# Kernel optimization log

Measured on AMD Instinct MI355X. Metric: run time of the kernel, lower is better.

Reference implementation:

```python
import jax, jax.numpy as jnp
import numpy as np

EMG_SAMPLE_RATE = 2000
ROLLOUT_FREQ = 50
LEFT_CTX = 32
RIGHT_CTX = 32
NUM_POSITION_STEPS = 2000  # in EMG samples
OUT_CH = 20


def _interp_linear(x, size, align_corners):
    """x: [..., L] -> [..., size]; matches torch F.interpolate(mode='linear')."""
    L = x.shape[-1]
    if align_corners:
        src = jnp.arange(size, dtype=jnp.float32) * ((L - 1) / max(size - 1, 1))
    else:
        src = (jnp.arange(size, dtype=jnp.float32) + 0.5) * (L / size) - 0.5
        src = jnp.clip(src, 0.0, L - 1)
    lo = jnp.floor(src).astype(jnp.int32)
    hi = jnp.minimum(lo + 1, L - 1)
    w = (src - lo.astype(jnp.float32)).astype(x.dtype)
    return x[..., lo] * (1 - w) + x[..., hi] * w


def setup_inputs() -> dict:
    key = jax.random.key(0)
    ks = jax.random.split(key, 8)
    B, C, T = 32, 16, 8000
    F, K, H = 512, 65, 512
    emg = jax.random.normal(ks[0], (B, C, T), jnp.float32)
    joint_angles = jax.random.normal(ks[1], (B, OUT_CH, T), jnp.float32)
    no_ik_failure = jnp.ones((B, T), dtype=bool)
    conv_w = jax.random.normal(ks[2], (F, C, K), jnp.float32) * 0.05
    conv_b = jnp.zeros((F,), jnp.float32)
    w1 = jax.random.normal(ks[3], (F + OUT_CH, H), jnp.float32) * 0.04
    b1 = jnp.zeros((H,), jnp.float32)
    w2 = jax.random.normal(ks[4], (H, 2 * OUT_CH), jnp.float32) * 0.04
    b2 = jnp.zeros((2 * OUT_CH,), jnp.float32)
    return dict(emg=emg, joint_angles=joint_angles, no_ik_failure=no_ik_failure,
                provide_initial_pos=1, conv_w=conv_w, conv_b=conv_b,
                w1=w1, b1=b1, w2=w2, b2=b2)


def reference(emg, joint_angles, no_ik_failure, provide_initial_pos,
              conv_w, conv_b, w1, b1, w2, b2):
    B, _, T = emg.shape
    initial_pos = joint_angles[:, :, LEFT_CTX]
    if not provide_initial_pos:
        initial_pos = jnp.zeros_like(initial_pos)

    # encoder: valid Conv1d -> [B, F, T - K + 1] = [B, F, T - 64]
    feats = jax.lax.conv_general_dilated(
        emg, conv_w, window_strides=(1,), padding='VALID',
        dimension_numbers=('NCH', 'OIH', 'NCH')) + conv_b[None, :, None]

    seconds = (T - LEFT_CTX - RIGHT_CTX) / EMG_SAMPLE_RATE
    n_time = round(seconds * ROLLOUT_FREQ)          # static python int
    feats = _interp_linear(feats, n_time, align_corners=True)  # [B, F, n_time]
    num_pos_steps = round(NUM_POSITION_STEPS * (ROLLOUT_FREQ / EMG_SAMPLE_RATE))

    feats_t = jnp.transpose(feats, (2, 0, 1))  # [n_time, B, F]

    def step(prev, inp):
        x_t, t = inp
        # state_condition=True: concat previous pose prediction
        h = jax.nn.relu(jnp.concatenate([x_t, prev], axis=-1) @ w1 + b1)
        out = h @ w2 + b2                       # [B, 2*OUT_CH]
        pos, vel = out[:, :OUT_CH], out[:, OUT_CH:]
        pred = jnp.where(t < num_pos_steps, pos, prev + vel)
        return pred, pred

    _, preds = jax.lax.scan(step, initial_pos,
                            (feats_t, jnp.arange(n_time)))
    pred = jnp.transpose(preds, (1, 2, 0))  # [B, OUT_CH, n_time]

    ja = joint_angles[:, :, LEFT_CTX:T - RIGHT_CTX]
    mask = no_ik_failure[:, LEFT_CTX:T - RIGHT_CTX]
    nt = ja.shape[-1]
    pred_up = _interp_linear(pred, nt, align_corners=False)
    # nearest resample of mask to its own length is identity
    return pred_up, ja, mask
```

## Files before the change

kernel.cpp:

```cpp
#include <hip/hip_runtime.h>

#define NT   198
#define BB   32
#define CC   16
#define TT   8000
#define FF   512
#define KW   65
#define HD   512
#define OUT  20
#define CJ   (CC*KW)
#define KP   1056
#define MM   (NT*BB)
#define TOUT 7936
#define NPS  50

typedef float f4 __attribute__((ext_vector_type(4)));

#define WS_CW 0
#define WS_BX (WS_CW + KP*HD)
#define WS_X  (WS_BX + HD)
#define WS_PR (WS_X  + MM*HD)
#define WS_ET (WS_PR + MM*OUT)
#define WS_W2T (WS_ET + KP*MM)

#define ESPAN 2688
__global__ __launch_bounds__(256) void k_e2(const float* __restrict__ emg,
                                            float* __restrict__ Et) {
    const int bx = blockIdx.x;
    const int tc = blockIdx.y;
    const int tid = threadIdx.x;
    if (bx >= BB * CC) {
        int idx = (bx - BB * CC) * 3 + tc;
        f4* zp = (f4*)(Et + (size_t)CJ * MM);
        f4 z = {0.f, 0.f, 0.f, 0.f};
        for (int j = tid; j < 2112; j += 256) zp[(size_t)idx * 2112 + j] = z;
        return;
    }
    __shared__ float lds_e[ESPAN];
    const int bq = bx >> 4, c = bx & 15;
    const int t0 = tc * 66;
    const float CSTEP = 7935.0f / 197.0f;
    const int elo0 = (int)floorf((float)t0 * CSTEP);
    const float* erow = emg + (size_t)(bq * CC + c) * TT;
    for (int i = tid; i < ESPAN; i += 256) {
        int g = elo0 + i;
        lds_e[i] = erow[(g < TT) ? g : (TT - 1)];
    }
    __syncthreads();
    for (int o = tid; o < 65 * 66; o += 256) {
        int j = o / 66;
        int tl = o - j * 66;
        int t = t0 + tl;
        float src = (float)t * CSTEP;
        float fl = floorf(src);
        int lo = (int)fl;
        float w = src - fl;
        int dhi = (w > 0.f && lo < TOUT - 1) ? 1 : 0;
        int li = lo - elo0 + j;
        float v = (1.0f - w) * lds_e[li] + w * lds_e[li + dhi];
        Et[(size_t)(c * KW + j) * MM + bq * NT + t] = v;
    }
}

__global__ __launch_bounds__(256) void k_cw2(const float* __restrict__ cwraw,
                                             const float* __restrict__ w1,
                                             float* __restrict__ CW) {
    __shared__ float As[32][68];
    __shared__ float Bs[32][68];
    const int m0 = blockIdx.x * 64;
    const int n0 = blockIdx.y * 64;
    const int tid = threadIdx.x;
    const int tx = tid & 15, ty = tid >> 4;
    const int am = tid & 63;
    const int kb8 = (tid >> 6) * 8;
    const int mrow = m0 + am;
    const int mclamp = mrow < CJ ? mrow : CJ - 1;

    f4 acc[4] = {};
    for (int k0 = 0; k0 < FF; k0 += 32) {
        __syncthreads();
        #pragma unroll
        for (int s = 0; s < 8; ++s)
            As[kb8 + s][am] = cwraw[(size_t)(k0 + kb8 + s) * CJ + mclamp];
        {
            int kb = tid >> 4, c4 = tid & 15;
            *(f4*)&Bs[kb][c4 * 4]      = *(const f4*)(w1 + (size_t)(k0 + kb) * HD + n0 + c4 * 4);
            *(f4*)&Bs[kb + 16][c4 * 4] = *(const f4*)(w1 + (size_t)(k0 + kb + 16) * HD + n0 + c4 * 4);
        }
        __syncthreads();
        #pragma unroll
        for (int kk = 0; kk < 32; ++kk) {
            f4 a = *(f4*)&As[kk][ty * 4];
            f4 bq = *(f4*)&Bs[kk][tx * 4];
            acc[0] += a[0] * bq; acc[1] += a[1] * bq;
            acc[2] += a[2] * bq; acc[3] += a[3] * bq;
        }
    }
    #pragma unroll
    for (int i = 0; i < 4; ++i) {
        int r = m0 + ty * 4 + i;
        if (r < CJ) {
            *(f4*)(CW + (size_t)r * HD + n0 + tx * 4) = acc[i];
        } else if (r < KP) {
            f4 z = {0.f, 0.f, 0.f, 0.f};
            *(f4*)(CW + (size_t)r * HD + n0 + tx * 4) = z;
        }
    }
}

__global__ __launch_bounds__(256) void k_small2(const float* __restrict__ conv_b,
                                                const float* __restrict__ w1,
                                                const float* __restrict__ b1,
                                                const float* __restrict__ w2,
                                                float* __restrict__ bX,
                                                float* __restrict__ w2t) {
    int bid = blockIdx.x, tid = threadIdx.x;
    if (bid < 2) {
        int h = bid * 256 + tid;
        float acc = b1[h];
        for (int f = 0; f < FF; ++f) acc += conv_b[f] * w1[f * HD + h];
        bX[h] = acc;
    } else {
        int q = bid - 2;
        w2t[(size_t)q * HD + tid]       = w2[(size_t)tid * (2 * OUT) + q];
        w2t[(size_t)q * HD + 256 + tid] = w2[(size_t)(256 + tid) * (2 * OUT) + q];
    }
}

__global__ __launch_bounds__(128) void k_x9(const float* __restrict__ Et,
                                            const float* __restrict__ CW,
                                            const float* __restrict__ bX,
                                            float* __restrict__ X0,
                                            float* __restrict__ X1,
                                            float* __restrict__ X2,
                                            float* __restrict__ X3) {
    __shared__ float As[32][68];
    __shared__ float Bs0[32][68];
    __shared__ float Bs1[32][68];
    const int m0 = blockIdx.x * 64;
    const int n0 = blockIdx.y * 128;
    const int kc = blockIdx.z;
    const int kbase = kc * 256;
    const int NK = (kc == 3) ? 9 : 8;
    const int tid = threadIdx.x;
    const int tm = tid >> 4;
    const int tn = tid & 15;
    const int akr = tid >> 4;
    const int ag  = tid & 15;
    const int bkr = tid >> 5;
    const int bg  = tid & 31;

    f4 acc0[8] = {}, acc1[8] = {};

    for (int kt = 0; kt < NK; ++kt) {
        const int k0 = kbase + kt * 32;
        __syncthreads();
        #pragma unroll
        for (int s = 0; s < 4; ++s) {
            f4 v = *(const f4*)(Et + (size_t)(k0 + akr + 8 * s) * MM + m0 + ag * 4);
            *(f4*)&As[akr + 8 * s][ag * 4] = v;
        }
        #pragma unroll
        for (int s = 0; s < 8; ++s) {
            int kr = bkr + 4 * s;
            f4 v = *(const f4*)(CW + (size_t)(k0 + kr) * HD + n0 + bg * 4);
            if (bg < 16) *(f4*)&Bs0[kr][bg * 4] = v;
            else         *(f4*)&Bs1[kr][(bg - 16) * 4] = v;
        }
        __syncthreads();
        #pragma unroll
        for (int kk = 0; kk < 32; ++kk) {
            f4 a0 = *(const f4*)&As[kk][tm * 8];
            f4 a1 = *(const f4*)&As[kk][tm * 8 + 4];
            f4 b0 = *(const f4*)&Bs0[kk][tn * 4];
            f4 b1 = *(const f4*)&Bs1[kk][tn * 4];
            #pragma unroll
            for (int i = 0; i < 4; ++i) {
                acc0[i]     += a0[i] * b0;  acc1[i]     += a0[i] * b1;
                acc0[i + 4] += a1[i] * b0;  acc1[i + 4] += a1[i] * b1;
            }
        }
    }

    float* Xo = (kc == 0) ? X0 : (kc == 1) ? X1 : (kc == 2) ? X2 : X3;
    if (kc == 0) {
        f4 bx0 = *(const f4*)(bX + n0 + tn * 4);
        f4 bx1 = *(const f4*)(bX + n0 + 64 + tn * 4);
        #pragma unroll
        for (int i = 0; i < 8; ++i) {
            size_t off = (size_t)(m0 + 8 * tm + i) * HD + n0;
            *(f4*)(Xo + off + tn * 4)      = acc0[i] + bx0;
            *(f4*)(Xo + off + 64 + tn * 4) = acc1[i] + bx1;
        }
    } else {
        #pragma unroll
        for (int i = 0; i < 8; ++i) {
            size_t off = (size_t)(m0 + 8 * tm + i) * HD + n0;
            *(f4*)(Xo + off + tn * 4)      = acc0[i];
            *(f4*)(Xo + off + 64 + tn * 4) = acc1[i];
        }
    }
}

__global__ __launch_bounds__(256) void k_sum(float* __restrict__ X0,
                                             const float* __restrict__ X1,
                                             const float* __restrict__ X2,
                                             const float* __restrict__ X3) {
    size_t i = (size_t)blockIdx.x * 256 + threadIdx.x;
    f4 a = ((const f4*)X0)[i];
    f4 b = ((const f4*)X1)[i];
    f4 c = ((const f4*)X2)[i];
    f4 d = ((const f4*)X3)[i];
    ((f4*)X0)[i] = (a + b) + (c + d);
}

#define DPPADD(x, ctrl) ((x) + __int_as_float(__builtin_amdgcn_mov_dpp(__float_as_int(x), (ctrl), 0xf, 0xf, true)))

#define SCAN_STEP(T, ISPOS) { \
    if (aown) { \
        int tp = (T) + 2; if (tp > NT - 1) tp = NT - 1; \
        float2 xf = *(const float2*)(Xr + (size_t)tp * HD); \
        f4 pp[5]; \
        _Pragma("unroll") \
        for (int g = 0; g < 5; ++g) pp[g] = *(const f4*)&prev_lds[(T) & 1][g * 4]; \
        float h0 = xc.x, h1 = xc.y; \
        _Pragma("unroll") \
        for (int j = 0; j < OUT; ++j) { \
            float pj = pp[j >> 2][j & 3]; \
            h0 = fmaf(pj, w1p[j].x, h0); h1 = fmaf(pj, w1p[j].y, h1); } \
        h0 = fmaxf(h0, 0.f); h1 = fmaxf(h1, 0.f); \
        float2 hw; hw.x = h0; hw.y = h1; \
        *(float2*)&h_lds[(T) & 1][tid >> 4][(2 * tid) & 31] = hw; \
        xc = xn; xn = xf; \
    } \
    __syncthreads(); \
    f4 a = {0.f, 0.f, 0.f, 0.f}; \
    _Pragma("unroll") \
    for (int s = 0; s < 8; ++s) { \
        f4 hv = *(const f4*)&h_lds[(T) & 1][r][s * 4]; \
        a += hv * ((ISPOS) ? wqp[s] : wqv[s]); } \
    float sum = (a[0] + a[1]) + (a[2] + a[3]); \
    sum = DPPADD(sum, 0xB1);    \
    sum = DPPADD(sum, 0x4E);    \
    sum = DPPADD(sum, 0x141);   \
    sum = DPPADD(sum, 0x140);   \
    float outv = sum + ((ISPOS) ? b2p : b2v); \
    myq = (ISPOS) ? outv : (myq + outv); \
    if (r == 0) { \
        predrow[(size_t)(T) * OUT + q] = myq; \
        prev_lds[((T) + 1) & 1][q] = myq; } \
    __syncthreads(); }

__global__ __launch_bounds__(320, 1) void k_scan(
        const float* __restrict__ X, const float* __restrict__ w1,
        const float* __restrict__ w2t, const float* __restrict__ b2,
        const float* __restrict__ jang, const int* __restrict__ provide,
        float* __restrict__ preds) {
    __shared__ float h_lds[2][16][36];
    __shared__ __align__(16) float prev_lds[2][20];
    const int b = blockIdx.x;
    const int tid = threadIdx.x;
    const int q = tid >> 4;
    const int r = tid & 15;
    const bool aown = tid < 256;

    float2 w1p[OUT];
    if (aown) {
        #pragma unroll
        for (int j = 0; j < OUT; ++j)
            w1p[j] = *(const float2*)(w1 + (size_t)(FF + j) * HD + 2 * tid);
    }
    f4 wqp[8], wqv[8];
    #pragma unroll
    for (int s = 0; s < 8; ++s) {
        wqp[s] = *(const f4*)(w2t + (size_t)q * HD + r * 32 + s * 4);
        wqv[s] = *(const f4*)(w2t + (size_t)(OUT + q) * HD + r * 32 + s * 4);
    }
    float b2p = b2[q], b2v = b2[OUT + q];

    float pvf = provide[0] ? 1.0f : 0.0f;
    float myq = pvf * jang[(size_t)(b * OUT + q) * TT + 32];
    if (r == 0) prev_lds[0][q] = myq;

    const float* Xr = X + (size_t)b * NT * HD + 2 * tid;
    float* predrow = preds + (size_t)b * NT * OUT;
    float2 xc = {0.f, 0.f}, xn = {0.f, 0.f};
    if (aown) {
        xc = *(const float2*)(Xr);
        xn = *(const float2*)(Xr + HD);
    }
    __syncthreads();

    for (int t = 0; t < NPS; ++t) { SCAN_STEP(t, true) }
    for (int t = NPS; t < NT; ++t) { SCAN_STEP(t, false) }
}

__global__ __launch_bounds__(256) void k_out(const float* __restrict__ preds,
                                             const float* __restrict__ jang,
                                             const unsigned char* __restrict__ m,
                                             float* __restrict__ outp) {
    __shared__ float row[NT];
    const int bid = blockIdx.x;
    const int tid = threadIdx.x;
    const int NF4 = TOUT / 4;
    if (bid < BB * OUT) {
        int rc = bid;
        int bq = rc / OUT, ch = rc - bq * OUT;
        if (tid < NT) row[tid] = preds[(size_t)(bq * NT + tid) * OUT + ch];
        __syncthreads();
        const float scale = (float)NT / (float)TOUT;
        f4* op = (f4*)(outp + (size_t)rc * TOUT);
        for (int i = tid; i < NF4; i += 256) {
            f4 o;
            #pragma unroll
            for (int e = 0; e < 4; ++e) {
                int idx = 4 * i + e;
                float src = ((float)idx + 0.5f) * scale - 0.5f;
                src = fminf(fmaxf(src, 0.0f), (float)(NT - 1));
                float fl = floorf(src);
                int lo = (int)fl;
                int hi = lo + 1; if (hi > NT - 1) hi = NT - 1;
                float w = src - fl;
                o[e] = row[lo] * (1.0f - w) + row[hi] * w;
            }
            op[i] = o;
        }
    } else if (bid < 2 * BB * OUT) {
        int rc = bid - BB * OUT;
        f4* op = (f4*)(outp + (size_t)BB * OUT * TOUT + (size_t)rc * TOUT);
        const f4* ip = (const f4*)(jang + (size_t)rc * TT + 32);
        for (int i = tid; i < NF4; i += 256) op[i] = ip[i];
    } else {
        int b = bid - 2 * BB * OUT;
        f4* op = (f4*)(outp + (size_t)2 * BB * OUT * TOUT + (size_t)b * TOUT);
        const uchar4* mp = (const uchar4*)(m + (size_t)b * TT + 32);
        for (int i = tid; i < NF4; i += 256) {
            uchar4 mv = mp[i];
            f4 o;
            o[0] = mv.x ? 1.0f : 0.0f; o[1] = mv.y ? 1.0f : 0.0f;
            o[2] = mv.z ? 1.0f : 0.0f; o[3] = mv.w ? 1.0f : 0.0f;
            op[i] = o;
        }
    }
}

extern "C" void kernel_launch(void* const* d_in, const int* in_sizes, int n_in,
                              void* d_out, int out_size, void* d_ws, size_t ws_size,
                              hipStream_t stream) {
    const float* emg     = (const float*)d_in[0];
    const float* jang    = (const float*)d_in[1];
    const unsigned char* msk = (const unsigned char*)d_in[2];
    const int*   provide = (const int*)d_in[3];
    const float* conv_w  = (const float*)d_in[4];
    const float* conv_b  = (const float*)d_in[5];
    const float* w1      = (const float*)d_in[6];
    const float* b1      = (const float*)d_in[7];
    const float* w2      = (const float*)d_in[8];
    const float* b2      = (const float*)d_in[9];
    float* out = (float*)d_out;
    float* ws  = (float*)d_ws;

    float* CW    = ws + WS_CW;
    float* bX    = ws + WS_BX;
    float* X0    = ws + WS_X;
    float* preds = ws + WS_PR;
    float* Et    = ws + WS_ET;
    float* w2t   = ws + WS_W2T;
    float* X1    = out;
    float* X2    = out + (size_t)MM * HD;
    float* X3    = out + (size_t)2 * MM * HD;

    hipLaunchKernelGGL(k_e2,    dim3(BB * CC + 4, 3), dim3(256), 0, stream, emg, Et);
    hipLaunchKernelGGL(k_cw2,   dim3((KP + 63) / 64, HD / 64), dim3(256), 0, stream, conv_w, w1, CW);
    hipLaunchKernelGGL(k_small2, dim3(42), dim3(256), 0, stream, conv_b, w1, b1, w2, bX, w2t);
    hipLaunchKernelGGL(k_x9,    dim3(MM / 64, HD / 128, 4), dim3(128), 0, stream,
                       Et, CW, bX, X0, X1, X2, X3);
    hipLaunchKernelGGL(k_sum,   dim3(MM * HD / 4 / 256), dim3(256), 0, stream, X0, X1, X2, X3);
    hipLaunchKernelGGL(k_scan,  dim3(BB), dim3(320), 0, stream,
                       X0, w1, w2t, b2, jang, provide, preds);
    hipLaunchKernelGGL(k_out,   dim3(2 * BB * OUT + BB), dim3(256), 0, stream,
                       preds, jang, msk, out);
}
```

Measured before the change: 294.7 us.

## Fuse setup kernels, overlap output copies with scan, split scan FMA chains

Merges the emg-interpolation, conv-weight GEMM and small bias/transpose kernels into one launch using a flat block index and shared LDS. Moves the joint-angle copy and mask-to-float conversion into extra blocks of the scan kernel, so they run on otherwise idle CUs during the serial recurrence. The leftover upsample becomes its own small kernel. Inside each scan step, the 20-term and 32-term dot products are split into two independent accumulators to shorten the dependency chain. The risks are that the copy blocks compete with the scan blocks for memory bandwidth, and that the fused prologue needs a larger shared allocation.

Measured after the change: 264.3 us. 10.3% less time.

```diff
diff --git a/kernel.cpp b/kernel.cpp
--- a/kernel.cpp
+++ b/kernel.cpp
@@ -24,106 +24,110 @@
 #define WS_W2T (WS_ET + KP*MM)
 
 #define ESPAN 2688
-__global__ __launch_bounds__(256) void k_e2(const float* __restrict__ emg,
-                                            float* __restrict__ Et) {
-    const int bx = blockIdx.x;
-    const int tc = blockIdx.y;
+#define NB_E  (3 * (BB * CC + 4))
+#define NB_CW (((KP + 63) / 64) * (HD / 64))
+__global__ __launch_bounds__(256) void k_pre(const float* __restrict__ emg,
+                                             const float* __restrict__ cwraw,
+                                             const float* __restrict__ w1,
+                                             const float* __restrict__ conv_b,
+                                             const float* __restrict__ b1,
+                                             const float* __restrict__ w2,
+                                             float* __restrict__ Et,
+                                             float* __restrict__ CW,
+                                             float* __restrict__ bX,
+                                             float* __restrict__ w2t) {
+    __shared__ float sh[2 * 32 * 68];
+    const int bid = blockIdx.x;
     const int tid = threadIdx.x;
-    if (bx >= BB * CC) {
-        int idx = (bx - BB * CC) * 3 + tc;
-        f4* zp = (f4*)(Et + (size_t)CJ * MM);
-        f4 z = {0.f, 0.f, 0.f, 0.f};
-        for (int j = tid; j < 2112; j += 256) zp[(size_t)idx * 2112 + j] = z;
-        return;
-    }
-    __shared__ float lds_e[ESPAN];
-    const int bq = bx >> 4, c = bx & 15;
-    const int t0 = tc * 66;
-    const float CSTEP = 7935.0f / 197.0f;
-    const int elo0 = (int)floorf((float)t0 * CSTEP);
-    const float* erow = emg + (size_t)(bq * CC + c) * TT;
-    for (int i = tid; i < ESPAN; i += 256) {
-        int g = elo0 + i;
-        lds_e[i] = erow[(g < TT) ? g : (TT - 1)];
-    }
-    __syncthreads();
-    for (int o = tid; o < 65 * 66; o += 256) {
-        int j = o / 66;
-        int tl = o - j * 66;
-        int t = t0 + tl;
-        float src = (float)t * CSTEP;
-        float fl = floorf(src);
-        int lo = (int)fl;
-        float w = src - fl;
-        int dhi = (w > 0.f && lo < TOUT - 1) ? 1 : 0;
-        int li = lo - elo0 + j;
-        float v = (1.0f - w) * lds_e[li] + w * lds_e[li + dhi];
-        Et[(size_t)(c * KW + j) * MM + bq * NT + t] = v;
-    }
-}
-
-__global__ __launch_bounds__(256) void k_cw2(const float* __restrict__ cwraw,
-                                             const float* __restrict__ w1,
-                                             float* __restrict__ CW) {
-    __shared__ float As[32][68];
-    __shared__ float Bs[32][68];
-    const int m0 = blockIdx.x * 64;
-    const int n0 = blockIdx.y * 64;
-    const int tid = threadIdx.x;
-    const int tx = tid & 15, ty = tid >> 4;
-    const int am = tid & 63;
-    const int kb8 = (tid >> 6) * 8;
-    const int mrow = m0 + am;
-    const int mclamp = mrow < CJ ? mrow : CJ - 1;
-
-    f4 acc[4] = {};
-    for (int k0 = 0; k0 < FF; k0 += 32) {
+
+    if (bid < NB_E) {
+        const int bx = bid % (BB * CC + 4);
+        const int tc = bid / (BB * CC + 4);
+        if (bx >= BB * CC) {
+            int idx = (bx - BB * CC) * 3 + tc;
+            f4* zp = (f4*)(Et + (size_t)CJ * MM);
+            f4 z = {0.f, 0.f, 0.f, 0.f};
+            for (int j = tid; j < 2112; j += 256) zp[(size_t)idx * 2112 + j] = z;
+            return;
+        }
+        float* lds_e = sh;
+        const int bq = bx >> 4, c = bx & 15;
+        const int t0 = tc * 66;
+        const float CSTEP = 7935.0f / 197.0f;
+        const int elo0 = (int)floorf((float)t0 * CSTEP);
+        const float* erow = emg + (size_t)(bq * CC + c) * TT;
+        for (int i = tid; i < ESPAN; i += 256) {
+            int g = elo0 + i;
+            lds_e[i] = erow[(g < TT) ? g : (TT - 1)];
+        }
         __syncthreads();
-        #pragma unroll
-        for (int s = 0; s < 8; ++s)
-            As[kb8 + s][am] = cwraw[(size_t)(k0 + kb8 + s) * CJ + mclamp];
-        {
-            int kb = tid >> 4, c4 = tid & 15;
-            *(f4*)&Bs[kb][c4 * 4]      = *(const f4*)(w1 + (size_t)(k0 + kb) * HD + n0 + c4 * 4);
-            *(f4*)&Bs[kb + 16][c4 * 4] = *(const f4*)(w1 + (size_t)(k0 + kb + 16) * HD + n0 + c4 * 4);
-        }
-        __syncthreads();
-        #pragma unroll
-        for (int kk = 0; kk < 32; ++kk) {
-            f4 a = *(f4*)&As[kk][ty * 4];
-            f4 bq = *(f4*)&Bs[kk][tx * 4];
-            acc[0] += a[0] * bq; acc[1] += a[1] * bq;
-            acc[2] += a[2] * bq; acc[3] += a[3] * bq;
-        }
-    }
-    #pragma unroll
-    for (int i = 0; i < 4; ++i) {
-        int r = m0 + ty * 4 + i;
-        if (r < CJ) {
-            *(f4*)(CW + (size_t)r * HD + n0 + tx * 4) = acc[i];
-        } else if (r < KP) {
-            f4 z = {0.f, 0.f, 0.f, 0.f};
-            *(f4*)(CW + (size_t)r * HD + n0 + tx * 4) = z;
-        }
-    }
-}
-
-__global__ __launch_bounds__(256) void k_small2(const float* __restrict__ conv_b,
-                                                const float* __restrict__ w1,
-                                                const float* __restrict__ b1,
-                                                const float* __restrict__ w2,
-                                                float* __restrict__ bX,
-                                                float* __restrict__ w2t) {
-    int bid = blockIdx.x, tid = threadIdx.x;
-    if (bid < 2) {
-        int h = bid * 256 + tid;
-        float acc = b1[h];
-        for (int f = 0; f < FF; ++f) acc += conv_b[f] * w1[f * HD + h];
-        bX[h] = acc;
+        for (int o = tid; o < 65 * 66; o += 256) {
+            int j = o / 66;
+            int tl = o - j * 66;
+            int t = t0 + tl;
+            float src = (float)t * CSTEP;
+            float fl = floorf(src);
+            int lo = (int)fl;
+            float w = src - fl;
+            int dhi = (w > 0.f && lo < TOUT - 1) ? 1 : 0;
+            int li = lo - elo0 + j;
+            float v = (1.0f - w) * lds_e[li] + w * lds_e[li + dhi];
+            Et[(size_t)(c * KW + j) * MM + bq * NT + t] = v;
+        }
+    } else if (bid < NB_E + NB_CW) {
+        const int cb = bid - NB_E;
+        const int m0 = (cb % 17) * 64;
+        const int n0 = (cb / 17) * 64;
+        float (*As)[68] = (float(*)[68])sh;
+        float (*Bs)[68] = (float(*)[68])(sh + 32 * 68);
+        const int tx = tid & 15, ty = tid >> 4;
+        const int am = tid & 63;
+        const int kb8 = (tid >> 6) * 8;
+        const int mrow = m0 + am;
+        const int mclamp = mrow < CJ ? mrow : CJ - 1;
+
+        f4 acc[4] = {};
+        for (int k0 = 0; k0 < FF; k0 += 32) {
+            __syncthreads();
+            #pragma unroll
+            for (int s = 0; s < 8; ++s)
+                As[kb8 + s][am] = cwraw[(size_t)(k0 + kb8 + s) * CJ + mclamp];
+            {
+                int kb = tid >> 4, c4 = tid & 15;
+                *(f4*)&Bs[kb][c4 * 4]      = *(const f4*)(w1 + (size_t)(k0 + kb) * HD + n0 + c4 * 4);
+                *(f4*)&Bs[kb + 16][c4 * 4] = *(const f4*)(w1 + (size_t)(k0 + kb + 16) * HD + n0 + c4 * 4);
+            }
+            __syncthreads();
+            #pragma unroll
+            for (int kk = 0; kk < 32; ++kk) {
+                f4 a = *(f4*)&As[kk][ty * 4];
+                f4 bq = *(f4*)&Bs[kk][tx * 4];
+                acc[0] += a[0] * bq; acc[1] += a[1] * bq;
+                acc[2] += a[2] * bq; acc[3] += a[3] * bq;
+            }
+        }
+        #pragma unroll
+        for (int i = 0; i < 4; ++i) {
+            int r = m0 + ty * 4 + i;
+            if (r < CJ) {
+                *(f4*)(CW + (size_t)r * HD + n0 + tx * 4) = acc[i];
+            } else if (r < KP) {
+                f4 z = {0.f, 0.f, 0.f, 0.f};
+                *(f4*)(CW + (size_t)r * HD + n0 + tx * 4) = z;
+            }
+        }
     } else {
-        int q = bid - 2;
-        w2t[(size_t)q * HD + tid]       = w2[(size_t)tid * (2 * OUT) + q];
-        w2t[(size_t)q * HD + 256 + tid] = w2[(size_t)(256 + tid) * (2 * OUT) + q];
+        const int sb = bid - NB_E - NB_CW;
+        if (sb < 2) {
+            int h = sb * 256 + tid;
+            float acc = b1[h];
+            for (int f = 0; f < FF; ++f) acc += conv_b[f] * w1[f * HD + h];
+            bX[h] = acc;
+        } else {
+            int q = sb - 2;
+            w2t[(size_t)q * HD + tid]       = w2[(size_t)tid * (2 * OUT) + q];
+            w2t[(size_t)q * HD + 256 + tid] = w2[(size_t)(256 + tid) * (2 * OUT) + q];
+        }
     }
 }
 
@@ -223,22 +227,29 @@
         f4 pp[5]; \
         _Pragma("unroll") \
         for (int g = 0; g < 5; ++g) pp[g] = *(const f4*)&prev_lds[(T) & 1][g * 4]; \
-        float h0 = xc.x, h1 = xc.y; \
+        float h0a = xc.x, h0b = 0.f, h1a = xc.y, h1b = 0.f; \
         _Pragma("unroll") \
-        for (int j = 0; j < OUT; ++j) { \
+        for (int j = 0; j < 10; ++j) { \
             float pj = pp[j >> 2][j & 3]; \
-            h0 = fmaf(pj, w1p[j].x, h0); h1 = fmaf(pj, w1p[j].y, h1); } \
-        h0 = fmaxf(h0, 0.f); h1 = fmaxf(h1, 0.f); \
+            h0a = fmaf(pj, w1p[j].x, h0a); h1a = fmaf(pj, w1p[j].y, h1a); } \
+        _Pragma("unroll") \
+        for (int j = 10; j < OUT; ++j) { \
+            float pj = pp[j >> 2][j & 3]; \
+            h0b = fmaf(pj, w1p[j].x, h0b); h1b = fmaf(pj, w1p[j].y, h1b); } \
+        float h0 = fmaxf(h0a + h0b, 0.f), h1 = fmaxf(h1a + h1b, 0.f); \
         float2 hw; hw.x = h0; hw.y = h1; \
         *(float2*)&h_lds[(T) & 1][tid >> 4][(2 * tid) & 31] = hw; \
         xc = xn; xn = xf; \
     } \
     __syncthreads(); \
-    f4 a = {0.f, 0.f, 0.f, 0.f}; \
+    f4 alo = {0.f, 0.f, 0.f, 0.f}, ahi = {0.f, 0.f, 0.f, 0.f}; \
     _Pragma("unroll") \
-    for (int s = 0; s < 8; ++s) { \
-        f4 hv = *(const f4*)&h_lds[(T) & 1][r][s * 4]; \
-        a += hv * ((ISPOS) ? wqp[s] : wqv[s]); } \
+    for (int s = 0; s < 4; ++s) { \
+        f4 hv0 = *(const f4*)&h_lds[(T) & 1][r][s * 4]; \
+        f4 hv1 = *(const f4*)&h_lds[(T) & 1][r][(s + 4) * 4]; \
+        alo += hv0 * ((ISPOS) ? wqp[s] : wqv[s]); \
+        ahi += hv1 * ((ISPOS) ? wqp[s + 4] : wqv[s + 4]); } \
+    f4 a = alo + ahi; \
     float sum = (a[0] + a[1]) + (a[2] + a[3]); \
     sum = DPPADD(sum, 0xB1);    \
     sum = DPPADD(sum, 0x4E);    \
@@ -255,11 +266,36 @@
         const float* __restrict__ X, const float* __restrict__ w1,
         const float* __restrict__ w2t, const float* __restrict__ b2,
         const float* __restrict__ jang, const int* __restrict__ provide,
-        float* __restrict__ preds) {
+        float* __restrict__ preds, const unsigned char* __restrict__ m,
+        float* __restrict__ outp) {
+    const int bid = blockIdx.x;
+    const int tid = threadIdx.x;
+    const int NF4 = TOUT / 4;
+
+    if (bid >= BB) {
+        int cb = bid - BB;
+        if (cb < BB * OUT) {
+            f4* op = (f4*)(outp + (size_t)BB * OUT * TOUT + (size_t)cb * TOUT);
+            const f4* ip = (const f4*)(jang + (size_t)cb * TT + 32);
+            for (int i = tid; i < NF4; i += 320) op[i] = ip[i];
+        } else {
+            int b = cb - BB * OUT;
+            f4* op = (f4*)(outp + (size_t)2 * BB * OUT * TOUT + (size_t)b * TOUT);
+            const uchar4* mp = (const uchar4*)(m + (size_t)b * TT + 32);
+            for (int i = tid; i < NF4; i += 320) {
+                uchar4 mv = mp[i];
+                f4 o;
+                o[0] = mv.x ? 1.0f : 0.0f; o[1] = mv.y ? 1.0f : 0.0f;
+                o[2] = mv.z ? 1.0f : 0.0f; o[3] = mv.w ? 1.0f : 0.0f;
+                op[i] = o;
+            }
+        }
+        return;
+    }
+
     __shared__ float h_lds[2][16][36];
     __shared__ __align__(16) float prev_lds[2][20];
-    const int b = blockIdx.x;
-    const int tid = threadIdx.x;
+    const int b = bid;
     const int q = tid >> 4;
     const int r = tid & 15;
     const bool aown = tid < 256;
@@ -295,52 +331,31 @@
     for (int t = NPS; t < NT; ++t) { SCAN_STEP(t, false) }
 }
 
-__global__ __launch_bounds__(256) void k_out(const float* __restrict__ preds,
-                                             const float* __restrict__ jang,
-                                             const unsigned char* __restrict__ m,
-                                             float* __restrict__ outp) {
+__global__ __launch_bounds__(256) void k_up(const float* __restrict__ preds,
+                                            float* __restrict__ outp) {
     __shared__ float row[NT];
-    const int bid = blockIdx.x;
+    const int rc = blockIdx.x;
     const int tid = threadIdx.x;
     const int NF4 = TOUT / 4;
-    if (bid < BB * OUT) {
-        int rc = bid;
-        int bq = rc / OUT, ch = rc - bq * OUT;
-        if (tid < NT) row[tid] = preds[(size_t)(bq * NT + tid) * OUT + ch];
-        __syncthreads();
-        const float scale = (float)NT / (float)TOUT;
-        f4* op = (f4*)(outp + (size_t)rc * TOUT);
-        for (int i = tid; i < NF4; i += 256) {
-            f4 o;
-            #pragma unroll
-            for (int e = 0; e < 4; ++e) {
-                int idx = 4 * i + e;
-                float src = ((float)idx + 0.5f) * scale - 0.5f;
-                src = fminf(fmaxf(src, 0.0f), (float)(NT - 1));
-                float fl = floorf(src);
-                int lo = (int)fl;
-                int hi = lo + 1; if (hi > NT - 1) hi = NT - 1;
-                float w = src - fl;
-                o[e] = row[lo] * (1.0f - w) + row[hi] * w;
-            }
-            op[i] = o;
-        }
-    } else if (bid < 2 * BB * OUT) {
-        int rc = bid - BB * OUT;
-        f4* op = (f4*)(outp + (size_t)BB * OUT * TOUT + (size_t)rc * TOUT);
-        const f4* ip = (const f4*)(jang + (size_t)rc * TT + 32);
-        for (int i = tid; i < NF4; i += 256) op[i] = ip[i];
-    } else {
-        int b = bid - 2 * BB * OUT;
-        f4* op = (f4*)(outp + (size_t)2 * BB * OUT * TOUT + (size_t)b * TOUT);
-        const uchar4* mp = (const uchar4*)(m + (size_t)b * TT + 32);
-        for (int i = tid; i < NF4; i += 256) {
-            uchar4 mv = mp[i];
-            f4 o;
-            o[0] = mv.x ? 1.0f : 0.0f; o[1] = mv.y ? 1.0f : 0.0f;
-            o[2] = mv.z ? 1.0f : 0.0f; o[3] = mv.w ? 1.0f : 0.0f;
-            op[i] = o;
-        }
+    int bq = rc / OUT, ch = rc - bq * OUT;
+    if (tid < NT) row[tid] = preds[(size_t)(bq * NT + tid) * OUT + ch];
+    __syncthreads();
+    const float scale = (float)NT / (float)TOUT;
+    f4* op = (f4*)(outp + (size_t)rc * TOUT);
+    for (int i = tid; i < NF4; i += 256) {
+        f4 o;
+        #pragma unroll
+        for (int e = 0; e < 4; ++e) {
+            int idx = 4 * i + e;
+            float src = ((float)idx + 0.5f) * scale - 0.5f;
+            src = fminf(fmaxf(src, 0.0f), (float)(NT - 1));
+            float fl = floorf(src);
+            int lo = (int)fl;
+            int hi = lo + 1; if (hi > NT - 1) hi = NT - 1;
+            float w = src - fl;
+            o[e] = row[lo] * (1.0f - w) + row[hi] * w;
+        }
+        op[i] = o;
     }
 }
 
@@ -370,14 +385,12 @@
     float* X2    = out + (size_t)MM * HD;
     float* X3    = out + (size_t)2 * MM * HD;
 
-    hipLaunchKernelGGL(k_e2,    dim3(BB * CC + 4, 3), dim3(256), 0, stream, emg, Et);
-    hipLaunchKernelGGL(k_cw2,   dim3((KP + 63) / 64, HD / 64), dim3(256), 0, stream, conv_w, w1, CW);
-    hipLaunchKernelGGL(k_small2, dim3(42), dim3(256), 0, stream, conv_b, w1, b1, w2, bX, w2t);
-    hipLaunchKernelGGL(k_x9,    dim3(MM / 64, HD / 128, 4), dim3(128), 0, stream,
+    hipLaunchKernelGGL(k_pre,  dim3(NB_E + NB_CW + 42), dim3(256), 0, stream,
+                       emg, conv_w, w1, conv_b, b1, w2, Et, CW, bX, w2t);
+    hipLaunchKernelGGL(k_x9,   dim3(MM / 64, HD / 128, 4), dim3(128), 0, stream,
                        Et, CW, bX, X0, X1, X2, X3);
-    hipLaunchKernelGGL(k_sum,   dim3(MM * HD / 4 / 256), dim3(256), 0, stream, X0, X1, X2, X3);
-    hipLaunchKernelGGL(k_scan,  dim3(BB), dim3(320), 0, stream,
-                       X0, w1, w2t, b2, jang, provide, preds);
-    hipLaunchKernelGGL(k_out,   dim3(2 * BB * OUT + BB), dim3(256), 0, stream,
-                       preds, jang, msk, out);
-}
+    hipLaunchKernelGGL(k_sum,  dim3(MM * HD / 4 / 256), dim3(256), 0, stream, X0, X1, X2, X3);
+    hipLaunchKernelGGL(k_scan, dim3(BB + 2 * BB * OUT + BB - BB * OUT), dim3(320), 0, stream,
+                       X0, w1, w2t, b2, jang, provide, preds, msk, out);
+    hipLaunchKernelGGL(k_up,   dim3(BB * OUT), dim3(256), 0, stream, preds, out);
+}
```
